# Kernel optimization log

Measured on AMD Instinct MI355X. Metric: run time of the kernel, lower is better.

## Reference

```python
import jax, jax.numpy as jnp
import numpy as np

H = 2048          # hidden_size
I = 2048          # per-expert intermediate = 6144 // (topk=2 + share=1)
E_ROUTED = 7      # num_experts - num_share_experts
NS = 1            # num_share_experts
TOPK = 2
TEMP = 1.0


def setup_inputs() -> dict:
    key = jax.random.key(0)
    ks = jax.random.split(key, 20)
    s = lambda fan_in: 1.0 / np.sqrt(fan_in)
    inp = {
        "x": jax.random.normal(ks[0], (4, 1024, H), dtype=jnp.float32),
        # router (nn.Linear(H, E_ROUTED)) + learnable gate bias (init zeros)
        "Wr": jax.random.normal(ks[1], (H, E_ROUTED), jnp.float32) * s(H),
        "br": jax.random.normal(ks[2], (E_ROUTED,), jnp.float32) * s(H),
        "gate_bias": jnp.zeros((E_ROUTED,), jnp.float32),
        # stacked routed-expert FFN params (up -> SwiGLU gate -> down)
        "Wup": jax.random.normal(ks[3], (E_ROUTED, H, I), jnp.float32) * s(H),
        "bup": jax.random.normal(ks[4], (E_ROUTED, I), jnp.float32) * s(H),
        "Wgate": jax.random.normal(ks[5], (E_ROUTED, I, I), jnp.float32) * s(I),
        "bgate": jax.random.normal(ks[6], (E_ROUTED, I), jnp.float32) * s(I),
        "Wdown": jax.random.normal(ks[7], (E_ROUTED, I, H), jnp.float32) * s(I),
        "bdown": jax.random.normal(ks[8], (E_ROUTED, H), jnp.float32) * s(I),
        # shared expert: share_up Linear(H, NS*I), SwiGLU(I), share_down Linear(I, H)
        "Wsu": jax.random.normal(ks[9], (H, NS * I), jnp.float32) * s(H),
        "bsu": jax.random.normal(ks[10], (NS * I,), jnp.float32) * s(H),
        "Wsg": jax.random.normal(ks[11], (I, I), jnp.float32) * s(I),
        "bsg": jax.random.normal(ks[12], (I,), jnp.float32) * s(I),
        "Wsd": jax.random.normal(ks[13], (I, H), jnp.float32) * s(I),
        "bsd": jax.random.normal(ks[14], (H,), jnp.float32) * s(I),
    }
    return inp


def _moe_forward(x, Wr, br, gate_bias, Wup, bup, Wgate, bgate, Wdown, bdown,
                 Wsu, bsu, Wsg, bsg, Wsd, bsd):
    B, S, _ = x.shape
    xt = x.reshape(-1, H)                                   # [N, H]
    N = xt.shape[0]

    # ---- router: top-k gating with scatter(-inf) + softmax over all routed experts
    gate = (xt @ Wr + br) / TEMP                            # [N, E]
    bias_gate = gate + gate_bias
    _, ids = jax.lax.top_k(bias_gate, TOPK)                 # [N, K]
    sel_logits = jnp.take_along_axis(gate, ids, axis=-1)    # [N, K] (unbiased logits)
    masked = jnp.full_like(gate, -jnp.inf)
    masked = masked.at[jnp.arange(N)[:, None], ids].set(sel_logits)
    probs = jax.nn.softmax(masked, axis=-1)                 # [N, E], zero off top-k

    # ---- routed experts: dense grouped FFN, combine weighted by probs
    # (probs are exactly 0 for unselected experts, matching the masked
    #  gather / scatter-add combine in the original loop)
    u = jnp.einsum('nh,ehi->eni', xt, Wup) + bup[:, None, :]            # [E, N, I]
    g = jax.nn.silu(jnp.einsum('eni,eij->enj', u, Wgate) + bgate[:, None, :]) * u
    eo = jnp.einsum('enj,ejh->enh', g, Wdown) + bdown[:, None, :]       # [E, N, H]
    out = jnp.einsum('ne,enh->nh', probs, eo)                           # [N, H]

    # ---- shared expert(s)
    su = (xt @ Wsu + bsu).reshape(N, NS, I)                 # [N, NS, I]
    sg = jax.nn.silu(su @ Wsg + bsg) * su                   # SwiGLU
    so = (sg @ Wsd + bsd).sum(axis=1)                       # [N, H]
    out = out + so

    return out.reshape(B, S, H)


def reference(x, Wr, br, gate_bias, Wup, bup, Wgate, bgate, Wdown, bdown,
              Wsu, bsu, Wsg, bsg, Wsd, bsd):
    return _moe_forward(x, Wr, br, gate_bias, Wup, bup, Wgate, bgate,
                        Wdown, bdown, Wsu, bsu, Wsg, bsg, Wsd, bsd)
```

## Files before the change

kernel.cpp:

```cpp
#include <hip/hip_runtime.h>
#include <stdint.h>

#define HD 2048
#define NTOK 4096
#define NROUTED 7
#define NEXP 8
#define ROWS_ROUTED 8192
#define ROWS_TOTAL 12288
#define ROWS_PAD 12416

typedef __attribute__((ext_vector_type(8))) __bf16 bf16x8;
typedef __attribute__((ext_vector_type(4))) float f32x4;
typedef __attribute__((ext_vector_type(8))) unsigned short u16x8;

__device__ __forceinline__ float bf2f(unsigned short h) {
  union { unsigned int u; float f; } x; x.u = ((unsigned int)h) << 16; return x.f;
}
__device__ __forceinline__ unsigned short f2bf(float f) {
  union { float f; unsigned int u; } x; x.f = f;
  unsigned int r = x.u + 0x7fffu + ((x.u >> 16) & 1u);
  return (unsigned short)(r >> 16);
}

__device__ __forceinline__ void async16(const void* g, void* l) {
  __builtin_amdgcn_global_load_lds(
      (__attribute__((address_space(1))) const void*)(uintptr_t)g,
      (__attribute__((address_space(3))) void*)(unsigned int)(uintptr_t)l,
      16, 0, 0);
}

__global__ __launch_bounds__(256) void k_convert_bf16(const float* __restrict__ in,
                                                      unsigned short* __restrict__ out, int n) {
  int i = (blockIdx.x * 256 + threadIdx.x) * 4;
  if (i >= n) return;
  float4 v = *(const float4*)(in + i);
  ushort4 o; o.x = f2bf(v.x); o.y = f2bf(v.y); o.z = f2bf(v.z); o.w = f2bf(v.w);
  *(ushort4*)(out + i) = o;
}

__global__ __launch_bounds__(256) void k_transpose_bf16(const float* __restrict__ in,
                                                        unsigned short* __restrict__ out) {
  __shared__ float tile[32][33];
  const size_t bs = (size_t)HD * HD;
  in += (size_t)blockIdx.z * bs; out += (size_t)blockIdx.z * bs;
  int x = threadIdx.x & 31, y = threadIdx.x >> 5;
  int r0 = blockIdx.y * 32, c0 = blockIdx.x * 32;
  #pragma unroll
  for (int i = 0; i < 4; i++) tile[y + 8*i][x] = in[(size_t)(r0 + y + 8*i) * HD + c0 + x];
  __syncthreads();
  #pragma unroll
  for (int i = 0; i < 4; i++) out[(size_t)(c0 + y + 8*i) * HD + r0 + x] = f2bf(tile[x][y + 8*i]);
}

__global__ __launch_bounds__(256) void k_router(const float* __restrict__ x, const float* __restrict__ Wr,
                                                const float* __restrict__ br, const float* __restrict__ gbias,
                                                int* __restrict__ ids, float* __restrict__ wts,
                                                int* __restrict__ ctrl) {
  int lane = threadIdx.x & 63, wid = threadIdx.x >> 6;
  int t = blockIdx.x * 4 + wid;
  const float* xr = x + (size_t)t * HD;
  float acc[NROUTED];
  #pragma unroll
  for (int e = 0; e < NROUTED; e++) acc[e] = 0.f;
  for (int k = lane; k < HD; k += 64) {
    float xv = xr[k];
    const float* wrow = Wr + k * NROUTED;
    #pragma unroll
    for (int e = 0; e < NROUTED; e++) acc[e] += xv * wrow[e];
  }
  #pragma unroll
  for (int e = 0; e < NROUTED; e++) {
    #pragma unroll
    for (int off = 32; off > 0; off >>= 1) acc[e] += __shfl_down(acc[e], off);
  }
  if (lane == 0) {
    float lg[NROUTED], bg[NROUTED];
    #pragma unroll
    for (int e = 0; e < NROUTED; e++) { lg[e] = acc[e] + br[e]; bg[e] = lg[e] + gbias[e]; }
    int i1 = 0;
    #pragma unroll
    for (int e = 1; e < NROUTED; e++) if (bg[e] > bg[i1]) i1 = e;
    int i2 = (i1 == 0) ? 1 : 0;
    #pragma unroll
    for (int e = 0; e < NROUTED; e++) if (e != i1 && bg[e] > bg[i2]) i2 = e;
    float l1 = lg[i1], l2 = lg[i2];
    float m = fmaxf(l1, l2);
    float p1 = __expf(l1 - m), p2 = __expf(l2 - m);
    float s = p1 + p2;
    ids[2*t] = i1; ids[2*t+1] = i2;
    wts[2*t] = p1 / s; wts[2*t+1] = p2 / s;
    atomicAdd(&ctrl[i1], 1); atomicAdd(&ctrl[i2], 1);
  }
}

__global__ void k_offsets(int* ctrl) {
  if (threadIdx.x == 0 && blockIdx.x == 0) {
    ctrl[7] = NTOK;
    int o = 0;
    #pragma unroll
    for (int e = 0; e < NEXP; e++) { ctrl[8 + e] = o; o += ctrl[e]; }
  }
}

__global__ __launch_bounds__(256) void k_build_lists(const int* __restrict__ ids, int* __restrict__ ctrl,
                                                     int* __restrict__ tok_list, int* __restrict__ tok_pos) {
  int t = blockIdx.x * 256 + threadIdx.x;
  if (t >= NTOK) return;
  #pragma unroll
  for (int j = 0; j < 2; j++) {
    int e = ids[2*t + j];
    int pos = ctrl[8 + e] + atomicAdd(&ctrl[16 + e], 1);
    tok_list[pos] = t;
    tok_pos[2*t + j] = pos;
  }
  tok_list[ROWS_ROUTED + t] = t;
}

template<int MODE>
__global__ __launch_bounds__(256) void k_moe_gemm(
    const unsigned short* __restrict__ Abase,
    const unsigned short* __restrict__ WTr,
    const unsigned short* __restrict__ WTs,
    const float* __restrict__ biasR,
    const float* __restrict__ biasS,
    const int* __restrict__ ctrl,
    const int* __restrict__ tok_list,
    const unsigned short* __restrict__ Uep,
    unsigned short* __restrict__ Out)
{
  const int e   = blockIdx.z;
  const int cnt = ctrl[e];
  const int m0  = blockIdx.y * 128;
  if (m0 >= cnt) return;
  const int off = ctrl[8 + e];
  const int n0  = blockIdx.x * 128;

  const unsigned short* W = (e < NROUTED) ? (WTr + (size_t)e * HD * HD) : WTs;
  const float* bias = (e < NROUTED) ? (biasR + e * HD) : biasS;

  __shared__ __align__(16) unsigned short As[128 * 32];
  __shared__ __align__(16) unsigned short Bs[128 * 32];

  const int tid  = threadIdx.x;
  const int lane = tid & 63;
  const int wid  = tid >> 6;

  const int srow = tid >> 2;
  const int skel = (tid & 3) * 8;

  int ar0 = m0 + srow, ar1 = m0 + 64 + srow;
  size_t ga0, ga1;
  if (MODE == 0) {
    int c1 = cnt - 1;
    int t0 = tok_list[off + (ar0 < cnt ? ar0 : c1)];
    int t1 = tok_list[off + (ar1 < cnt ? ar1 : c1)];
    ga0 = (size_t)t0 * HD; ga1 = (size_t)t1 * HD;
  } else {
    ga0 = (size_t)(off + ar0) * HD; ga1 = (size_t)(off + ar1) * HD;
  }
  const unsigned short* pA0 = Abase + ga0 + skel;
  const unsigned short* pA1 = Abase + ga1 + skel;
  const unsigned short* pB0 = W + (size_t)(n0 + srow) * HD + skel;
  const unsigned short* pB1 = W + (size_t)(n0 + 64 + srow) * HD + skel;

  unsigned short* lA0 = As + wid * 512;
  unsigned short* lA1 = As + 2048 + wid * 512;
  unsigned short* lB0 = Bs + wid * 512;
  unsigned short* lB1 = Bs + 2048 + wid * 512;

  const int wm = (wid >> 1) * 64;
  const int wn = (wid & 1) * 64;
  const int rm = lane & 15;
  const int kq = (lane >> 4) * 8;

  f32x4 zero = {0.f, 0.f, 0.f, 0.f};
  f32x4 acc[4][4];
  #pragma unroll
  for (int i = 0; i < 4; i++)
    #pragma unroll
    for (int j = 0; j < 4; j++) acc[i][j] = zero;

  for (int k0 = 0; k0 < HD; k0 += 32) {
    __syncthreads();
    async16(pA0, lA0); async16(pA1, lA1);
    async16(pB0, lB0); async16(pB1, lB1);
    pA0 += 32; pA1 += 32; pB0 += 32; pB1 += 32;
    __syncthreads();
    bf16x8 af[4], bfr[4];
    #pragma unroll
    for (int mi = 0; mi < 4; mi++) af[mi]  = *(const bf16x8*)(As + (wm + mi*16 + rm) * 32 + kq);
    #pragma unroll
    for (int ni = 0; ni < 4; ni++) bfr[ni] = *(const bf16x8*)(Bs + (wn + ni*16 + rm) * 32 + kq);
    #pragma unroll
    for (int mi = 0; mi < 4; mi++)
      #pragma unroll
      for (int ni = 0; ni < 4; ni++)
        acc[mi][ni] = __builtin_amdgcn_mfma_f32_16x16x32_bf16(af[mi], bfr[ni], acc[mi][ni], 0, 0, 0);
  }

  const int quad = lane >> 4;
  #pragma unroll
  for (int mi = 0; mi < 4; mi++) {
    int rb = wm + mi * 16 + quad * 4;
    #pragma unroll
    for (int r = 0; r < 4; r++) {
      int gm = m0 + rb + r;
      if (gm < cnt) {
        size_t orow = (size_t)(off + gm) * HD;
        #pragma unroll
        for (int ni = 0; ni < 4; ni++) {
          int gn = n0 + wn + ni * 16 + rm;
          float v = acc[mi][ni][r] + bias[gn];
          if (MODE == 1) {
            float uv = bf2f(Uep[orow + gn]);
            float sg = v / (1.f + __expf(-v));
            v = sg * uv;
          }
          Out[orow + gn] = f2bf(v);
        }
      }
    }
  }
}

__global__ __launch_bounds__(256) void k_combine(const unsigned short* __restrict__ eo,
                                                 const int* __restrict__ tok_pos,
                                                 const float* __restrict__ wts,
                                                 float* __restrict__ out) {
  int t = blockIdx.x;
  int h = threadIdx.x * 8;
  int p0 = tok_pos[2*t], p1 = tok_pos[2*t+1];
  float w0 = wts[2*t], w1 = wts[2*t+1];
  u16x8 a = *(const u16x8*)(eo + (size_t)p0 * HD + h);
  u16x8 b = *(const u16x8*)(eo + (size_t)p1 * HD + h);
  u16x8 c = *(const u16x8*)(eo + (size_t)(ROWS_ROUTED + t) * HD + h);
  float* o = out + (size_t)t * HD + h;
  #pragma unroll
  for (int i = 0; i < 8; i++) o[i] = w0 * bf2f(a[i]) + w1 * bf2f(b[i]) + bf2f(c[i]);
}

extern "C" void kernel_launch(void* const* d_in, const int* in_sizes, int n_in,
                              void* d_out, int out_size, void* d_ws, size_t ws_size,
                              hipStream_t stream) {
  (void)in_sizes; (void)n_in; (void)out_size; (void)ws_size;
  const float* x     = (const float*)d_in[0];
  const float* Wr    = (const float*)d_in[1];
  const float* br    = (const float*)d_in[2];
  const float* gbias = (const float*)d_in[3];
  const float* Wup   = (const float*)d_in[4];
  const float* bup   = (const float*)d_in[5];
  const float* Wgate = (const float*)d_in[6];
  const float* bgate = (const float*)d_in[7];
  const float* Wdown = (const float*)d_in[8];
  const float* bdown = (const float*)d_in[9];
  const float* Wsu   = (const float*)d_in[10];
  const float* bsu   = (const float*)d_in[11];
  const float* Wsg   = (const float*)d_in[12];
  const float* bsg   = (const float*)d_in[13];
  const float* Wsd   = (const float*)d_in[14];
  const float* bsd   = (const float*)d_in[15];
  float* out = (float*)d_out;

  char* ws = (char*)d_ws;
  size_t o = 0;
  auto alloc = [&](size_t bytes) { char* p = ws + o; o += (bytes + 255) & ~(size_t)255; return p; };
  unsigned short* WT_r = (unsigned short*)alloc((size_t)7 * HD * HD * 2);
  unsigned short* WT_s = (unsigned short*)alloc((size_t)HD * HD * 2);
  unsigned short* xbf  = (unsigned short*)alloc((size_t)NTOK * HD * 2);
  unsigned short* bufU = (unsigned short*)alloc((size_t)ROWS_PAD * HD * 2);
  unsigned short* bufG = (unsigned short*)alloc((size_t)ROWS_PAD * HD * 2);
  int*   ctrl     = (int*)alloc(4096);
  int*   ids      = (int*)alloc(NTOK * 2 * 4);
  float* wts      = (float*)alloc(NTOK * 2 * 4);
  int*   tok_list = (int*)alloc(ROWS_TOTAL * 4);
  int*   tok_pos  = (int*)alloc(NTOK * 2 * 4);

  hipMemsetAsync(ctrl, 0, 96, stream);
  k_convert_bf16<<<NTOK * HD / 1024, 256, 0, stream>>>(x, xbf, NTOK * HD);
  k_router<<<NTOK / 4, 256, 0, stream>>>(x, Wr, br, gbias, ids, wts, ctrl);
  k_offsets<<<1, 64, 0, stream>>>(ctrl);
  k_build_lists<<<NTOK / 256, 256, 0, stream>>>(ids, ctrl, tok_list, tok_pos);

  dim3 tgrid(HD / 32, HD / 32, 7), tgrid1(HD / 32, HD / 32, 1);
  dim3 ggrid(HD / 128, 32, 8);

  k_transpose_bf16<<<tgrid, 256, 0, stream>>>(Wup, WT_r);
  k_transpose_bf16<<<tgrid1, 256, 0, stream>>>(Wsu, WT_s);
  k_moe_gemm<0><<<ggrid, 256, 0, stream>>>(xbf, WT_r, WT_s, bup, bsu, ctrl, tok_list, nullptr, bufU);

  k_transpose_bf16<<<tgrid, 256, 0, stream>>>(Wgate, WT_r);
  k_transpose_bf16<<<tgrid1, 256, 0, stream>>>(Wsg, WT_s);
  k_moe_gemm<1><<<ggrid, 256, 0, stream>>>(bufU, WT_r, WT_s, bgate, bsg, ctrl, tok_list, bufU, bufG);

  k_transpose_bf16<<<tgrid, 256, 0, stream>>>(Wdown, WT_r);
  k_transpose_bf16<<<tgrid1, 256, 0, stream>>>(Wsd, WT_s);
  k_moe_gemm<2><<<ggrid, 256, 0, stream>>>(bufG, WT_r, WT_s, bdown, bsd, ctrl, tok_list, nullptr, bufU);

  k_combine<<<NTOK, 256, 0, stream>>>(bufU, tok_pos, wts, out);
}
```

Baseline: 1.099 ms.

## Enlarge MoE GEMM tiles to 256x256 with double-buffered swizzled LDS

The grouped expert GEMM now uses 256x256 output tiles, 512 threads per block and eight waves, each holding a 128x64 accumulator. LDS is double-buffered so the async global-to-LDS load of the next K slice overlaps the MFMAs on the current one, with one barrier per iteration. An XOR swizzle on the 16-byte chunks avoids LDS bank conflicts. The weight transpose also moves to 64x64 tiles with float4 loads and ushort4 stores. Costs are higher register and LDS use per block (64KB, launch bounds 512,2) and more padded work on ragged expert row counts.

```diff
diff --git a/kernel.cpp b/kernel.cpp
--- a/kernel.cpp
+++ b/kernel.cpp
@@ -9,6 +9,11 @@
 #define ROWS_TOTAL 12288
 #define ROWS_PAD 12416
 
+#define BM 256
+#define BN 256
+#define BK 32
+#define NT (HD / BK)
+
 typedef __attribute__((ext_vector_type(8))) __bf16 bf16x8;
 typedef __attribute__((ext_vector_type(4))) float f32x4;
 typedef __attribute__((ext_vector_type(8))) unsigned short u16x8;
@@ -40,16 +45,31 @@
 
 __global__ __launch_bounds__(256) void k_transpose_bf16(const float* __restrict__ in,
                                                         unsigned short* __restrict__ out) {
-  __shared__ float tile[32][33];
+  __shared__ float tile[64][65];
   const size_t bs = (size_t)HD * HD;
   in += (size_t)blockIdx.z * bs; out += (size_t)blockIdx.z * bs;
-  int x = threadIdx.x & 31, y = threadIdx.x >> 5;
-  int r0 = blockIdx.y * 32, c0 = blockIdx.x * 32;
-  #pragma unroll
-  for (int i = 0; i < 4; i++) tile[y + 8*i][x] = in[(size_t)(r0 + y + 8*i) * HD + c0 + x];
+  int tx = threadIdx.x & 15, ty = threadIdx.x >> 4;
+  int r0 = blockIdx.y * 64, c0 = blockIdx.x * 64;
+  #pragma unroll
+  for (int i = 0; i < 4; i++) {
+    float4 v = *(const float4*)(in + (size_t)(r0 + ty + 16 * i) * HD + c0 + tx * 4);
+    tile[ty + 16 * i][tx * 4 + 0] = v.x;
+    tile[ty + 16 * i][tx * 4 + 1] = v.y;
+    tile[ty + 16 * i][tx * 4 + 2] = v.z;
+    tile[ty + 16 * i][tx * 4 + 3] = v.w;
+  }
   __syncthreads();
   #pragma unroll
-  for (int i = 0; i < 4; i++) out[(size_t)(c0 + y + 8*i) * HD + r0 + x] = f2bf(tile[x][y + 8*i]);
+  for (int i = 0; i < 4; i++) {
+    int orow = ty + 16 * i;
+    int oc = tx * 4;
+    ushort4 o;
+    o.x = f2bf(tile[oc + 0][orow]);
+    o.y = f2bf(tile[oc + 1][orow]);
+    o.z = f2bf(tile[oc + 2][orow]);
+    o.w = f2bf(tile[oc + 3][orow]);
+    *(ushort4*)(out + (size_t)(c0 + orow) * HD + r0 + oc) = o;
+  }
 }
 
 __global__ __launch_bounds__(256) void k_router(const float* __restrict__ x, const float* __restrict__ Wr,
@@ -116,8 +136,18 @@
   tok_list[ROWS_ROUTED + t] = t;
 }
 
+
+#define STAGE(bufp)                                                       \
+  { unsigned short* _a = &sm[bufp][0][0];                                 \
+    unsigned short* _b = &sm[bufp][1][0];                                 \
+    _Pragma("unroll")                                                     \
+    for (int r = 0; r < 2; r++) {                                         \
+      async16(pA[r], _a + r * 4096 + wid * 512); pA[r] += BK;             \
+      async16(pB[r], _b + r * 4096 + wid * 512); pB[r] += BK;             \
+    } }
+
 template<int MODE>
-__global__ __launch_bounds__(256) void k_moe_gemm(
+__global__ __launch_bounds__(512, 2) void k_moe_gemm(
     const unsigned short* __restrict__ Abase,
     const unsigned short* __restrict__ WTr,
     const unsigned short* __restrict__ WTs,
@@ -130,78 +160,82 @@
 {
   const int e   = blockIdx.z;
   const int cnt = ctrl[e];
-  const int m0  = blockIdx.y * 128;
+  const int m0  = blockIdx.y * BM;
   if (m0 >= cnt) return;
   const int off = ctrl[8 + e];
-  const int n0  = blockIdx.x * 128;
+  const int n0  = blockIdx.x * BN;
 
   const unsigned short* W = (e < NROUTED) ? (WTr + (size_t)e * HD * HD) : WTs;
   const float* bias = (e < NROUTED) ? (biasR + e * HD) : biasS;
 
-  __shared__ __align__(16) unsigned short As[128 * 32];
-  __shared__ __align__(16) unsigned short Bs[128 * 32];
+  __shared__ __align__(16) unsigned short sm[2][2][BM * BK];
 
   const int tid  = threadIdx.x;
   const int lane = tid & 63;
   const int wid  = tid >> 6;
 
-  const int srow = tid >> 2;
-  const int skel = (tid & 3) * 8;
-
-  int ar0 = m0 + srow, ar1 = m0 + 64 + srow;
-  size_t ga0, ga1;
-  if (MODE == 0) {
-    int c1 = cnt - 1;
-    int t0 = tok_list[off + (ar0 < cnt ? ar0 : c1)];
-    int t1 = tok_list[off + (ar1 < cnt ? ar1 : c1)];
-    ga0 = (size_t)t0 * HD; ga1 = (size_t)t1 * HD;
-  } else {
-    ga0 = (size_t)(off + ar0) * HD; ga1 = (size_t)(off + ar1) * HD;
-  }
-  const unsigned short* pA0 = Abase + ga0 + skel;
-  const unsigned short* pA1 = Abase + ga1 + skel;
-  const unsigned short* pB0 = W + (size_t)(n0 + srow) * HD + skel;
-  const unsigned short* pB1 = W + (size_t)(n0 + 64 + srow) * HD + skel;
-
-  unsigned short* lA0 = As + wid * 512;
-  unsigned short* lA1 = As + 2048 + wid * 512;
-  unsigned short* lB0 = Bs + wid * 512;
-  unsigned short* lB1 = Bs + 2048 + wid * 512;
-
-  const int wm = (wid >> 1) * 64;
-  const int wn = (wid & 1) * 64;
-  const int rm = lane & 15;
-  const int kq = (lane >> 4) * 8;
-
+  const int sc  = tid & 3;
+  const int rl  = tid >> 2;
+  const int csw = (sc ^ (rl & 3)) * 8;
+  const unsigned short* pA[2];
+  const unsigned short* pB[2];
+  #pragma unroll
+  for (int r = 0; r < 2; r++) {
+    int row = r * 128 + rl;
+    size_t ga;
+    if (MODE == 0) {
+      int mr = m0 + row; if (mr >= cnt) mr = cnt - 1;
+      ga = (size_t)tok_list[off + mr] * HD;
+    } else {
+      ga = (size_t)(off + m0 + row) * HD;
+    }
+    pA[r] = Abase + ga + csw;
+    pB[r] = W + (size_t)(n0 + row) * HD + csw;
+  }
+
+  const int wr   = wid >> 2;
+  const int wc   = wid & 3;
+  const int rm   = lane & 15;
+  const int q    = lane >> 4;
+  const int sw   = rm & 3;
+  const int aRow = wr * 128 + rm;
+  const int bRow = wc * 64 + rm;
+
+  f32x4 acc[8][4];
   f32x4 zero = {0.f, 0.f, 0.f, 0.f};
-  f32x4 acc[4][4];
-  #pragma unroll
-  for (int i = 0; i < 4; i++)
+  #pragma unroll
+  for (int i = 0; i < 8; i++)
     #pragma unroll
     for (int j = 0; j < 4; j++) acc[i][j] = zero;
 
-  for (int k0 = 0; k0 < HD; k0 += 32) {
-    __syncthreads();
-    async16(pA0, lA0); async16(pA1, lA1);
-    async16(pB0, lB0); async16(pB1, lB1);
-    pA0 += 32; pA1 += 32; pB0 += 32; pB1 += 32;
-    __syncthreads();
-    bf16x8 af[4], bfr[4];
-    #pragma unroll
-    for (int mi = 0; mi < 4; mi++) af[mi]  = *(const bf16x8*)(As + (wm + mi*16 + rm) * 32 + kq);
-    #pragma unroll
-    for (int ni = 0; ni < 4; ni++) bfr[ni] = *(const bf16x8*)(Bs + (wn + ni*16 + rm) * 32 + kq);
-    #pragma unroll
-    for (int mi = 0; mi < 4; mi++)
+  STAGE(0);
+  __syncthreads();
+
+  for (int t = 0; t < NT; ++t) {
+    const int buf = t & 1;
+    if (t + 1 < NT) STAGE(buf ^ 1);
+
+    const unsigned short* _ab = &sm[buf][0][0];
+    const unsigned short* _bb = &sm[buf][1][0];
+    bf16x8 af[8], bf[4];
+    #pragma unroll
+    for (int mi = 0; mi < 8; mi++)
+      af[mi] = *(const bf16x8*)(_ab + (aRow + mi * 16) * BK + ((q ^ sw) * 8));
+    #pragma unroll
+    for (int ni = 0; ni < 4; ni++)
+      bf[ni] = *(const bf16x8*)(_bb + (bRow + ni * 16) * BK + ((q ^ sw) * 8));
+    #pragma unroll
+    for (int mi = 0; mi < 8; mi++)
       #pragma unroll
       for (int ni = 0; ni < 4; ni++)
-        acc[mi][ni] = __builtin_amdgcn_mfma_f32_16x16x32_bf16(af[mi], bfr[ni], acc[mi][ni], 0, 0, 0);
-  }
-
-  const int quad = lane >> 4;
-  #pragma unroll
-  for (int mi = 0; mi < 4; mi++) {
-    int rb = wm + mi * 16 + quad * 4;
+        acc[mi][ni] = __builtin_amdgcn_mfma_f32_16x16x32_bf16(af[mi], bf[ni], acc[mi][ni], 0, 0, 0);
+
+    __syncthreads();
+  }
+
+  #pragma unroll
+  for (int mi = 0; mi < 8; mi++) {
+    int rb = wr * 128 + mi * 16 + q * 4;
     #pragma unroll
     for (int r = 0; r < 4; r++) {
       int gm = m0 + rb + r;
@@ -209,7 +243,7 @@
         size_t orow = (size_t)(off + gm) * HD;
         #pragma unroll
         for (int ni = 0; ni < 4; ni++) {
-          int gn = n0 + wn + ni * 16 + rm;
+          int gn = n0 + wc * 64 + ni * 16 + rm;
           float v = acc[mi][ni][r] + bias[gn];
           if (MODE == 1) {
             float uv = bf2f(Uep[orow + gn]);
@@ -281,20 +315,20 @@
   k_offsets<<<1, 64, 0, stream>>>(ctrl);
   k_build_lists<<<NTOK / 256, 256, 0, stream>>>(ids, ctrl, tok_list, tok_pos);
 
-  dim3 tgrid(HD / 32, HD / 32, 7), tgrid1(HD / 32, HD / 32, 1);
-  dim3 ggrid(HD / 128, 32, 8);
+  dim3 tgrid(HD / 64, HD / 64, 7), tgrid1(HD / 64, HD / 64, 1);
+  dim3 ggrid(HD / BN, 16, NEXP);
 
   k_transpose_bf16<<<tgrid, 256, 0, stream>>>(Wup, WT_r);
   k_transpose_bf16<<<tgrid1, 256, 0, stream>>>(Wsu, WT_s);
-  k_moe_gemm<0><<<ggrid, 256, 0, stream>>>(xbf, WT_r, WT_s, bup, bsu, ctrl, tok_list, nullptr, bufU);
+  k_moe_gemm<0><<<ggrid, 512, 0, stream>>>(xbf, WT_r, WT_s, bup, bsu, ctrl, tok_list, nullptr, bufU);
 
   k_transpose_bf16<<<tgrid, 256, 0, stream>>>(Wgate, WT_r);
   k_transpose_bf16<<<tgrid1, 256, 0, stream>>>(Wsg, WT_s);
-  k_moe_gemm<1><<<ggrid, 256, 0, stream>>>(bufU, WT_r, WT_s, bgate, bsg, ctrl, tok_list, bufU, bufG);
+  k_moe_gemm<1><<<ggrid, 512, 0, stream>>>(bufU, WT_r, WT_s, bgate, bsg, ctrl, tok_list, bufU, bufG);
 
   k_transpose_bf16<<<tgrid, 256, 0, stream>>>(Wdown, WT_r);
   k_transpose_bf16<<<tgrid1, 256, 0, stream>>>(Wsd, WT_s);
-  k_moe_gemm<2><<<ggrid, 256, 0, stream>>>(bufG, WT_r, WT_s, bdown, bsd, ctrl, tok_list, nullptr, bufU);
+  k_moe_gemm<2><<<ggrid, 512, 0, stream>>>(bufG, WT_r, WT_s, bdown, bsd, ctrl, tok_list, nullptr, bufU);
 
   k_combine<<<NTOK, 256, 0, stream>>>(bufU, tok_pos, wts, out);
 }
```

Result: slower. 1.215 ms (+10.6%).
